# Kernel optimization log

Hardware: AMD Instinct MI355X
Metric: run time of the kernel (lower is better)

The kernel has to match this reference:

```python
import jax, jax.numpy as jnp
import numpy as np

B, L, H, V, HALF = 128, 4096, 64, 64, 32
ALPHA = 0.95
LN_EPS = 1e-5


def _normalize(x):
    # torch F.normalize(dim=-1): x / max(||x||_2, 1e-12)
    n = jnp.linalg.norm(x, axis=-1, keepdims=True)
    return x / jnp.maximum(n, 1e-12)


def setup_inputs() -> dict:
    key = jax.random.key(0)
    ks = jax.random.split(key, 17)
    s = 0.05
    return {
        "seq": jax.random.randint(ks[0], (B, L), 0, V),
        "embed": jax.random.normal(ks[1], (V, H), jnp.float32),
        "W1": jax.random.normal(ks[2], (H, 2 * H), jnp.float32) * s,
        "b1": jnp.zeros((2 * H,), jnp.float32),
        "W2": jax.random.normal(ks[3], (2 * H, H), jnp.float32) * s,
        "b2": jnp.zeros((H,), jnp.float32),
        "gamma": jnp.ones((H,), jnp.float32),
        "beta": jnp.zeros((H,), jnp.float32),
        "Ws": jax.random.normal(ks[4], (H, HALF), jnp.float32) * s,
        "bs": jnp.zeros((HALF,), jnp.float32),
        "We": jax.random.normal(ks[5], (H, HALF), jnp.float32) * s,
        "be": jnp.zeros((HALF,), jnp.float32),
        "Wrp": jax.random.normal(ks[6], (2 * HALF, H), jnp.float32) * s,
        "brp": jnp.zeros((H,), jnp.float32),
        "Wout": jax.random.normal(ks[7], (H, V), jnp.float32) * s,
        "bout": jnp.zeros((V,), jnp.float32),
    }


def _forward(seq, embed, W1, b1, W2, b2, gamma, beta,
             Ws, bs, We, be, Wrp, brp, Wout, bout):
    # Encoder: embed + FF(ReLU) residual + LayerNorm
    h0 = embed[seq]                                   # [B,L,H]
    ff = jnp.maximum(h0 @ W1 + b1, 0.0) @ W2 + b2
    x = h0 + ff
    mu = x.mean(-1, keepdims=True)
    var = ((x - mu) ** 2).mean(-1, keepdims=True)
    h = (x - mu) / jnp.sqrt(var + LN_EPS) * gamma + beta  # [B,L,H]

    # Precompute per-step projections for t = 0 .. L-2
    hp = h[:, :-1, :]                                 # [B,L-1,H]
    hs = hp @ Ws + bs                                 # [B,L-1,HALF]
    he = hp @ We + be
    ksn = _normalize(hs)
    ken = _normalize(he)
    scale = (jnp.arange(L - 1, dtype=h.dtype) + 1.0) / L  # (t+1)/L

    def step(carry, inp):
        M_s, M_e = carry                              # [B,HALF,HALF]
        hs_t, he_t, ks_t, ke_t, sc = inp
        vps = jnp.einsum('bij,bj->bi', M_s, ks_t)
        vpe = jnp.einsum('bij,bj->bi', M_e, ke_t)
        M_s = M_s + (1.0 - ALPHA) * (hs_t - vps)[:, :, None] * ks_t[:, None, :]
        M_e = M_e + (1.0 - ALPHA) * sc * (he_t - vpe)[:, :, None] * ke_t[:, None, :]
        return (M_s, M_e), None

    xs = (jnp.swapaxes(hs, 0, 1), jnp.swapaxes(he, 0, 1),
          jnp.swapaxes(ksn, 0, 1), jnp.swapaxes(ken, 0, 1), scale)
    M0 = jnp.zeros((B, HALF, HALF), h.dtype)
    (M_s, M_e), _ = jax.lax.scan(step, (M0, M0), xs)

    # Read with last-token query
    q = h[:, -1, :]
    qs = _normalize(q @ Ws + bs)
    qe = _normalize(q @ We + be)
    rs = jnp.einsum('bij,bj->bi', M_s, qs)
    re = jnp.einsum('bij,bj->bi', M_e, qe)
    r = jnp.concatenate([rs, re], axis=-1)            # [B,2*HALF]
    return (r @ Wrp + brp) @ Wout + bout              # [B,V]


def reference(seq, embed, W1, b1, W2, b2, gamma, beta,
              Ws, bs, We, be, Wrp, brp, Wout, bout):
    return _forward(seq, embed, W1, b1, W2, b2, gamma, beta,
                    Ws, bs, We, be, Wrp, brp, Wout, bout)
```

## Files before the change

kernel.cpp:

```cpp
#include <hip/hip_runtime.h>
#include <hip/hip_bf16.h>
#include <stdint.h>


#define BETA 0.05f
#define NB 128
#define NL 4096
#define TC 16
#define NCH 256
#define NBLD 6
#define SLOT_F 336
#define NSLOT 12

#define L_GR   (NSLOT * SLOT_F)
#define L_DA   (L_GR + 4096)
#define L_RV   (L_DA + 64)
#define L_O1   (L_RV + 64)
#define L_WHO  (L_O1 + 64)
#define L_TOT  (L_WHO + 1)

struct Ptrs { const void* p[15]; };

__device__ inline float readlane_f(float v, int l) {
    return __int_as_float(__builtin_amdgcn_readlane(__float_as_int(v), l));
}
__device__ inline float bperm_f(int idx, float v) {
    return __int_as_float(__builtin_amdgcn_ds_bpermute(idx, __float_as_int(v)));
}
__device__ inline float ldT(const float* p, int i) { return p[i]; }
__device__ inline float ldT(const __hip_bfloat16* p, int i) { return __bfloat162float(p[i]); }

template <typename T>
__device__ void build_tables_body(const T* emb, const T* W1, const T* b1,
                                  const T* W2, const T* b2, const T* gam,
                                  const T* bet, const T* Wsm, const T* bsv,
                                  const T* Wem, const T* bev, float* tbl)
{
    int v = blockIdx.x;
    int j = threadIdx.x;
    __shared__ float h0s[64];
    __shared__ float act[128];
    __shared__ float hrow[64];

    float h0 = ldT(emb, v * 64 + j);
    h0s[j] = h0;
    __syncthreads();

    float za = ldT(b1, j);
    float zb = ldT(b1, j + 64);
    for (int k = 0; k < 64; ++k) {
        float hk = h0s[k];
        za = fmaf(hk, ldT(W1, k * 128 + j), za);
        zb = fmaf(hk, ldT(W1, k * 128 + j + 64), zb);
    }
    act[j] = fmaxf(za, 0.0f);
    act[j + 64] = fmaxf(zb, 0.0f);
    __syncthreads();

    float ff = ldT(b2, j);
    for (int k = 0; k < 128; ++k)
        ff = fmaf(act[k], ldT(W2, k * 64 + j), ff);
    float x = h0 + ff;

    float s = x;
    for (int off = 32; off >= 1; off >>= 1) s += __shfl_xor(s, off, 64);
    float mu = s * (1.0f / 64.0f);
    float d = x - mu;
    float s2 = d * d;
    for (int off = 32; off >= 1; off >>= 1) s2 += __shfl_xor(s2, off, 64);
    float var = s2 * (1.0f / 64.0f);
    float h = d / sqrtf(var + 1e-5f) * ldT(gam, j) + ldT(bet, j);
    hrow[j] = h;
    __syncthreads();

    if (j < 32) {
        float sv = ldT(bsv, j);
        for (int k = 0; k < 64; ++k)
            sv = fmaf(hrow[k], ldT(Wsm, k * 32 + j), sv);
        float n2 = sv * sv;
        for (int off = 16; off >= 1; off >>= 1) n2 += __shfl_xor(n2, off, 64);
        float nrm = fmaxf(sqrtf(n2), 1e-12f);
        tbl[v * 32 + j] = sv;
        tbl[2048 + v * 32 + j] = sv / nrm;
    } else {
        int jj = j - 32;
        float ev = ldT(bev, jj);
        for (int k = 0; k < 64; ++k)
            ev = fmaf(hrow[k], ldT(Wem, k * 32 + jj), ev);
        float n2 = ev * ev;
        for (int off = 16; off >= 1; off >>= 1) n2 += __shfl_xor(n2, off, 64);
        float nrm = fmaxf(sqrtf(n2), 1e-12f);
        tbl[4096 + v * 32 + jj] = ev;
        tbl[6144 + v * 32 + jj] = ev / nrm;
    }
}

__global__ __launch_bounds__(64, 2) void build_tables(Ptrs ps, float* __restrict__ tbl,
                                                      int* __restrict__ flags)
{
    if (blockIdx.x == 0) {
        flags[threadIdx.x] = 0;
        flags[threadIdx.x + 64] = 0;
    }
    uint32_t g0 = *(const uint32_t*)ps.p[5];
    if (g0 == 0x3F803F80u)
        build_tables_body((const __hip_bfloat16*)ps.p[0], (const __hip_bfloat16*)ps.p[1],
                          (const __hip_bfloat16*)ps.p[2], (const __hip_bfloat16*)ps.p[3],
                          (const __hip_bfloat16*)ps.p[4], (const __hip_bfloat16*)ps.p[5],
                          (const __hip_bfloat16*)ps.p[6], (const __hip_bfloat16*)ps.p[7],
                          (const __hip_bfloat16*)ps.p[8], (const __hip_bfloat16*)ps.p[9],
                          (const __hip_bfloat16*)ps.p[10], tbl);
    else
        build_tables_body((const float*)ps.p[0], (const float*)ps.p[1],
                          (const float*)ps.p[2], (const float*)ps.p[3],
                          (const float*)ps.p[4], (const float*)ps.p[5],
                          (const float*)ps.p[6], (const float*)ps.p[7],
                          (const float*)ps.p[8], (const float*)ps.p[9],
                          (const float*)ps.p[10], tbl);
}

__global__ __launch_bounds__(512, 1) void ema_ms(
    const int* __restrict__ seq, const float* __restrict__ tbl,
    Ptrs ps, float* __restrict__ rvbuf, int* __restrict__ flags,
    void* __restrict__ outv)
{
    __shared__ float S[L_TOT];

    int bm = blockIdx.x;
    int b = bm >> 1, mat = bm & 1;
    int tid = threadIdx.x;
    int wid = tid >> 6, lane = tid & 63;
    const float bstep = BETA / 4096.0f;

    if (tid < 64) S[L_DA + tid] = 0.0f;

    const float* ktab = tbl + 2048 + mat * 4096;
    for (int i = tid; i < 2048; i += 512)
        S[(i >> 5) * 33 + (i & 31)] = ktab[i];
    __syncthreads();

    {
        float Kown[32];
#pragma unroll
        for (int j = 0; j < 32; ++j) Kown[j] = S[lane * 33 + j];
        for (int v8 = 0; v8 < 8; ++v8) {
            int vt = wid * 8 + v8;
            float acc = 0.0f;
#pragma unroll
            for (int j = 0; j < 32; ++j)
                acc = fmaf(S[vt * 33 + j], Kown[j], acc);
            S[L_GR + vt * 64 + lane] = acc;
        }
    }
    __syncthreads();

    const int* sb = seq + (size_t)b * NL;
    float y = 0.0f;
    if (wid == 0) {
        int vlast = sb[NL - 1];
        y = S[L_GR + vlast * 64 + lane];
    }

    const int NRND = (NCH + NBLD - 1) / NBLD;

    for (int r = 0; r <= NRND; ++r) {
        if (wid != 0 && wid != 4) {
            int bi = (wid > 4) ? (wid - 2) : (wid - 1);
            int ci = NBLD * r + bi;
            if (r < NRND && ci < NCH) {
                int c = NCH - 1 - ci;
                float* slot = S + ((r & 1) * NBLD + bi) * SLOT_F;
                int tokv = 0; float bneg = 0.0f;
                if (lane < TC) {
                    int t = c * TC + (TC - 1) - lane;
                    tokv = sb[t];
                    float bb = mat ? bstep * (float)(t + 1) : BETA;
                    if (t == NL - 1) bb = 0.0f;
                    bneg = -bb;
                    ((int*)(slot + 320))[lane] = tokv;
                }
                float garr[TC];
#pragma unroll
                for (int p = 0; p < TC; ++p) {
                    int vp = __builtin_amdgcn_readlane(tokv, p);
                    garr[p] = S[L_GR + vp * 64 + tokv] * bneg;
                }
                float x[TC];
                x[0] = (lane == 0) ? 1.0f : 0.0f;
#pragma unroll
                for (int p = 1; p < TC; ++p) {
                    float xp = (lane == p) ? 1.0f : 0.0f;
#pragma unroll
                    for (int j = 0; j < p; ++j)
                        xp = fmaf(readlane_f(garr[p], j), x[j], xp);
                    x[p] = xp;
                }
                if (lane < TC) {
#pragma unroll
                    for (int p = 0; p < TC; ++p)
                        slot[p * 20 + lane] = x[p];
                }
            }
        } else if (wid == 0 && r >= 1) {
            int rpar = ((r - 1) & 1) * NBLD;
            int base_ci = NBLD * (r - 1);
            int nch_r = NCH - base_ci;
            if (nch_r > NBLD) nch_r = NBLD;

            float* slot0 = S + rpar * SLOT_F;
            int tokc = ((int*)(slot0 + 320))[lane & 15];
            const float4* vr0 = (const float4*)(slot0 + (lane & 15) * 20);
            float4 Vc0 = vr0[0], Vc1 = vr0[1], Vc2 = vr0[2], Vc3 = vr0[3];
            float gpc[16];
#pragma unroll
            for (int p = 0; p < 16; ++p) {
                int vp = __builtin_amdgcn_readlane(tokc, p);
                gpc[p] = S[L_GR + vp * 64 + lane];
            }

            for (int bi = 0; bi < nch_r; ++bi) {
                int ci = base_ci + bi;
                int c = NCH - 1 - ci;
                float ry = bperm_f(tokc << 2, y);

                int tokn = 0;
                float4 Vn0, Vn1, Vn2, Vn3;
                float gpn[16];
                bool hasn = (bi + 1 < nch_r);
                if (hasn) {
                    float* slotn = S + (rpar + bi + 1) * SLOT_F;
                    tokn = ((int*)(slotn + 320))[lane & 15];
                    const float4* vr = (const float4*)(slotn + (lane & 15) * 20);
                    Vn0 = vr[0]; Vn1 = vr[1]; Vn2 = vr[2]; Vn3 = vr[3];
#pragma unroll
                    for (int p = 0; p < 16; ++p) {
                        int vp = __builtin_amdgcn_readlane(tokn, p);
                        gpn[p] = S[L_GR + vp * 64 + lane];
                    }
                }
                asm volatile("" ::: "memory");

                float bv = 0.0f;
                if (lane < TC) {
                    int t = c * TC + (TC - 1) - lane;
                    float bb = mat ? bstep * (float)(t + 1) : BETA;
                    if (t == NL - 1) bb = 0.0f;
                    bv = bb;
                }
                float s0 = Vc0.x * readlane_f(ry, 0);
                float s1 = Vc0.y * readlane_f(ry, 1);
                float s2 = Vc0.z * readlane_f(ry, 2);
                float s3 = Vc0.w * readlane_f(ry, 3);
                s0 = fmaf(Vc1.x, readlane_f(ry, 4), s0);
                s1 = fmaf(Vc1.y, readlane_f(ry, 5), s1);
                s2 = fmaf(Vc1.z, readlane_f(ry, 6), s2);
                s3 = fmaf(Vc1.w, readlane_f(ry, 7), s3);
                s0 = fmaf(Vc2.x, readlane_f(ry, 8), s0);
                s1 = fmaf(Vc2.y, readlane_f(ry, 9), s1);
                s2 = fmaf(Vc2.z, readlane_f(ry, 10), s2);
                s3 = fmaf(Vc2.w, readlane_f(ry, 11), s3);
                s0 = fmaf(Vc3.x, readlane_f(ry, 12), s0);
                s1 = fmaf(Vc3.y, readlane_f(ry, 13), s1);
                s2 = fmaf(Vc3.z, readlane_f(ry, 14), s2);
                s3 = fmaf(Vc3.w, readlane_f(ry, 15), s3);
                float dv = ((s0 + s1) + (s2 + s3)) * bv;
                if (lane < TC) atomicAdd(&S[L_DA + tokc], dv);
                float dn = -dv;
                float ya = 0.f, yb = 0.f, yc2 = 0.f, yd = 0.f;
#pragma unroll
                for (int p = 0; p < TC; p += 4) {
                    ya  = fmaf(readlane_f(dn, p),     gpc[p],     ya);
                    yb  = fmaf(readlane_f(dn, p + 1), gpc[p + 1], yb);
                    yc2 = fmaf(readlane_f(dn, p + 2), gpc[p + 2], yc2);
                    yd  = fmaf(readlane_f(dn, p + 3), gpc[p + 3], yd);
                }
                y += (ya + yb) + (yc2 + yd);

                if (hasn) {
                    tokc = tokn;
                    Vc0 = Vn0; Vc1 = Vn1; Vc2 = Vn2; Vc3 = Vn3;
#pragma unroll
                    for (int p = 0; p < 16; ++p) gpc[p] = gpn[p];
                }
            }
        }
        __syncthreads();
    }

    if (tid < 32) {
        float rr = 0.0f;
        const float* hsrc = tbl + mat * 4096;
        for (int v = 0; v < 64; ++v)
            rr = fmaf(S[L_DA + v], hsrc[v * 32 + tid], rr);
        __hip_atomic_store(&rvbuf[bm * 32 + tid], rr,
                           __ATOMIC_RELAXED, __HIP_MEMORY_SCOPE_AGENT);
    }
    __syncthreads();
    if (tid == 0) {
        int old = __hip_atomic_fetch_add(&flags[b], 1,
                                         __ATOMIC_ACQ_REL, __HIP_MEMORY_SCOPE_AGENT);
        ((int*)S)[L_WHO] = old;
    }
    __syncthreads();
    if (((int*)S)[L_WHO] != 1) return;

    if (tid < 64)
        S[L_RV + tid] = __hip_atomic_load(&rvbuf[b * 64 + tid],
                                          __ATOMIC_RELAXED, __HIP_MEMORY_SCOPE_AGENT);
    __syncthreads();

    uint32_t g0h = *(const uint32_t*)ps.p[5];
    int isbf = (g0h == 0x3F803F80u) ? 1 : 0;
    if (tid < 64) {
        float o;
        if (isbf) {
            const __hip_bfloat16* W = (const __hip_bfloat16*)ps.p[11];
            o = __bfloat162float(((const __hip_bfloat16*)ps.p[12])[tid]);
            for (int i = 0; i < 64; ++i)
                o = fmaf(S[L_RV + i], __bfloat162float(W[i * 64 + tid]), o);
        } else {
            const float* W = (const float*)ps.p[11];
            o = ((const float*)ps.p[12])[tid];
            for (int i = 0; i < 64; ++i)
                o = fmaf(S[L_RV + i], W[i * 64 + tid], o);
        }
        S[L_O1 + tid] = o;
    }
    __syncthreads();
    if (tid < 64) {
        float o2;
        if (isbf) {
            const __hip_bfloat16* W = (const __hip_bfloat16*)ps.p[13];
            o2 = __bfloat162float(((const __hip_bfloat16*)ps.p[14])[tid]);
            for (int i = 0; i < 64; ++i)
                o2 = fmaf(S[L_O1 + i], __bfloat162float(W[i * 64 + tid]), o2);
            ((__hip_bfloat16*)outv)[b * 64 + tid] = __float2bfloat16(o2);
        } else {
            const float* W = (const float*)ps.p[13];
            o2 = ((const float*)ps.p[14])[tid];
            for (int i = 0; i < 64; ++i)
                o2 = fmaf(S[L_O1 + i], W[i * 64 + tid], o2);
            ((float*)outv)[b * 64 + tid] = o2;
        }
    }
}

extern "C" void kernel_launch(void* const* d_in, const int* in_sizes, int n_in,
                              void* d_out, int out_size, void* d_ws, size_t ws_size,
                              hipStream_t stream) {
    const int* seq = (const int*)d_in[0];
    Ptrs ps;
    for (int i = 0; i < 15; ++i) ps.p[i] = d_in[i + 1];

    float* tbl = (float*)d_ws;
    float* rvbuf = tbl + 8192;
    int* flags = (int*)(rvbuf + 8192);

    build_tables<<<64, 64, 0, stream>>>(ps, tbl, flags);
    ema_ms<<<NB * 2, 512, 0, stream>>>(seq, tbl, ps, rvbuf, flags, d_out);
}
```

Baseline: 215.0 us.

## Stage gathered G rows into slot buffers by builder waves; simplify serial prefetch

Builder waves now copy the 16 gathered Gram rows for each chunk into an enlarged LDS slot, so the serial wave 0 reads them contiguously instead of doing indirect gathers by token. The next-chunk prefetch becomes unconditional, clamping to the current slot on the last chunk, which removes branches from the critical loop. The LDS atomicAdd is moved after the y update, so the serial dependency chain does not wait on it. Each slot grows from 336 to 1360 floats, which raises LDS use per block and may reduce occupancy.

New measurement: 195.6 us. 1.1x faster.

```diff
diff --git a/kernel.cpp b/kernel.cpp
--- a/kernel.cpp
+++ b/kernel.cpp
@@ -9,7 +9,7 @@
 #define TC 16
 #define NCH 256
 #define NBLD 6
-#define SLOT_F 336
+#define SLOT_F 1360
 #define NSLOT 12
 
 #define L_GR   (NSLOT * SLOT_F)
@@ -177,13 +177,15 @@
                     float bb = mat ? bstep * (float)(t + 1) : BETA;
                     if (t == NL - 1) bb = 0.0f;
                     bneg = -bb;
-                    ((int*)(slot + 320))[lane] = tokv;
+                    ((int*)(slot + 1344))[lane] = tokv;
                 }
                 float garr[TC];
 #pragma unroll
                 for (int p = 0; p < TC; ++p) {
                     int vp = __builtin_amdgcn_readlane(tokv, p);
-                    garr[p] = S[L_GR + vp * 64 + tokv] * bneg;
+                    const float* gr = S + L_GR + vp * 64;
+                    slot[320 + p * 64 + lane] = gr[lane];
+                    garr[p] = gr[tokv] * bneg;
                 }
                 float x[TC];
                 x[0] = (lane == 0) ? 1.0f : 0.0f;
@@ -208,38 +210,29 @@
             if (nch_r > NBLD) nch_r = NBLD;
 
             float* slot0 = S + rpar * SLOT_F;
-            int tokc = ((int*)(slot0 + 320))[lane & 15];
+            int tokc = ((int*)(slot0 + 1344))[lane & 15];
             const float4* vr0 = (const float4*)(slot0 + (lane & 15) * 20);
             float4 Vc0 = vr0[0], Vc1 = vr0[1], Vc2 = vr0[2], Vc3 = vr0[3];
             float gpc[16];
 #pragma unroll
-            for (int p = 0; p < 16; ++p) {
-                int vp = __builtin_amdgcn_readlane(tokc, p);
-                gpc[p] = S[L_GR + vp * 64 + lane];
-            }
+            for (int p = 0; p < 16; ++p)
+                gpc[p] = slot0[320 + p * 64 + lane];
 
             for (int bi = 0; bi < nch_r; ++bi) {
-                int ci = base_ci + bi;
-                int c = NCH - 1 - ci;
+                int c = NCH - 1 - (base_ci + bi);
+
+                int bin = (bi + 1 < nch_r) ? (bi + 1) : bi;
+                float* slotn = S + (rpar + bin) * SLOT_F;
+                int tokn = ((int*)(slotn + 1344))[lane & 15];
+                const float4* vrn = (const float4*)(slotn + (lane & 15) * 20);
+                float4 Vn0 = vrn[0], Vn1 = vrn[1], Vn2 = vrn[2], Vn3 = vrn[3];
+                float gpn[16];
+#pragma unroll
+                for (int p = 0; p < 16; ++p)
+                    gpn[p] = slotn[320 + p * 64 + lane];
+                asm volatile("" ::: "memory");
+
                 float ry = bperm_f(tokc << 2, y);
-
-                int tokn = 0;
-                float4 Vn0, Vn1, Vn2, Vn3;
-                float gpn[16];
-                bool hasn = (bi + 1 < nch_r);
-                if (hasn) {
-                    float* slotn = S + (rpar + bi + 1) * SLOT_F;
-                    tokn = ((int*)(slotn + 320))[lane & 15];
-                    const float4* vr = (const float4*)(slotn + (lane & 15) * 20);
-                    Vn0 = vr[0]; Vn1 = vr[1]; Vn2 = vr[2]; Vn3 = vr[3];
-#pragma unroll
-                    for (int p = 0; p < 16; ++p) {
-                        int vp = __builtin_amdgcn_readlane(tokn, p);
-                        gpn[p] = S[L_GR + vp * 64 + lane];
-                    }
-                }
-                asm volatile("" ::: "memory");
-
                 float bv = 0.0f;
                 if (lane < TC) {
                     int t = c * TC + (TC - 1) - lane;
@@ -264,7 +257,6 @@
                 s2 = fmaf(Vc3.z, readlane_f(ry, 14), s2);
                 s3 = fmaf(Vc3.w, readlane_f(ry, 15), s3);
                 float dv = ((s0 + s1) + (s2 + s3)) * bv;
-                if (lane < TC) atomicAdd(&S[L_DA + tokc], dv);
                 float dn = -dv;
                 float ya = 0.f, yb = 0.f, yc2 = 0.f, yd = 0.f;
 #pragma unroll
@@ -275,13 +267,12 @@
                     yd  = fmaf(readlane_f(dn, p + 3), gpc[p + 3], yd);
                 }
                 y += (ya + yb) + (yc2 + yd);
-
-                if (hasn) {
-                    tokc = tokn;
-                    Vc0 = Vn0; Vc1 = Vn1; Vc2 = Vn2; Vc3 = Vn3;
-#pragma unroll
-                    for (int p = 0; p < 16; ++p) gpc[p] = gpn[p];
-                }
+                if (lane < TC) atomicAdd(&S[L_DA + tokc], dv);
+
+                tokc = tokn;
+                Vc0 = Vn0; Vc1 = Vn1; Vc2 = Vn2; Vc3 = Vn3;
+#pragma unroll
+                for (int p = 0; p < 16; ++p) gpc[p] = gpn[p];
             }
         }
         __syncthreads();
```
